# Optimization experiments

Measured on AMD Instinct MI355X. Metric: run time of the kernel, lower is better.

The kernel has to match this reference:

```python
import jax, jax.numpy as jnp
import numpy as np

D_MODEL = 512
NUM_HEADS = 8
D_HEAD = D_MODEL // NUM_HEADS
B, S = 2, 4096


def setup_inputs() -> dict:
    key = jax.random.key(0)
    ks = jax.random.split(key, 9)
    scale = 1.0 / np.sqrt(D_MODEL)
    x = jax.random.normal(ks[0], (B, S, D_MODEL), dtype=jnp.float32)
    Wq = jax.random.normal(ks[1], (D_MODEL, D_MODEL), dtype=jnp.float32) * scale
    Wk = jax.random.normal(ks[2], (D_MODEL, D_MODEL), dtype=jnp.float32) * scale
    Wv = jax.random.normal(ks[3], (D_MODEL, D_MODEL), dtype=jnp.float32) * scale
    Wo = jax.random.normal(ks[4], (D_MODEL, D_MODEL), dtype=jnp.float32) * scale
    bq = jnp.zeros((D_MODEL,), jnp.float32)
    bk = jnp.zeros((D_MODEL,), jnp.float32)
    bv = jnp.zeros((D_MODEL,), jnp.float32)
    bo = jnp.zeros((D_MODEL,), jnp.float32)
    return {"x": x, "Wq": Wq, "bq": bq, "Wk": Wk, "bk": bk,
            "Wv": Wv, "bv": bv, "Wo": Wo, "bo": bo}


def _split_heads(t):
    # [B, S, D] -> [B, H, S, d_head]
    b, s, _ = t.shape
    return t.reshape(b, s, NUM_HEADS, D_HEAD).transpose(0, 2, 1, 3)


def reference(x, Wq, bq, Wk, bk, Wv, bv, Wo, bo):
    q = _split_heads(x @ Wq + bq)  # [B,H,S,dh]
    k = _split_heads(x @ Wk + bk)
    v = _split_heads(x @ Wv + bv)
    scores = jnp.einsum("bhqd,bhkd->bhqk", q, k) / jnp.sqrt(
        jnp.asarray(D_HEAD, x.dtype))
    attn = jax.nn.softmax(scores, axis=-1)  # dropout is identity at inference
    out = jnp.einsum("bhqk,bhkd->bhqd", attn, v)  # [B,H,S,dh]
    out = out.transpose(0, 2, 1, 3).reshape(x.shape[0], x.shape[1], D_MODEL)
    return out @ Wo + bo
```

## Files before the change

### kernel.cpp

```cpp
#include <hip/hip_runtime.h>
#include <cstddef>

#define NB   2
#define SEQ  4096
#define DM   512
#define NH   8
#define DH   64
#define MTOT 8192
#define KSPLIT 2
#define KSEQ (SEQ / KSPLIT)

#define QSCALE 0.18033688011112042f

typedef __attribute__((ext_vector_type(8))) short short8;
typedef __attribute__((ext_vector_type(4))) float f32x4;

__device__ __forceinline__ ushort f2bf(float f) {
  unsigned u = __builtin_bit_cast(unsigned, f);
  u += 0x7FFFu + ((u >> 16) & 1u);
  return (ushort)(u >> 16);
}
__device__ __forceinline__ float bf2f(ushort b) {
  return __builtin_bit_cast(float, ((unsigned)b) << 16);
}
__device__ __forceinline__ unsigned cvt_pk_bf16(float lo, float hi) {
  unsigned r;
  asm("v_cvt_pk_bf16_f32 %0, %1, %2" : "=v"(r) : "v"(lo), "v"(hi));
  return r;
}
__device__ __forceinline__ float fexp2(float x) {
#if __has_builtin(__builtin_amdgcn_exp2f)
  return __builtin_amdgcn_exp2f(x);
#else
  float r;
  asm("v_exp_f32 %0, %1" : "=v"(r) : "v"(x));
  return r;
#endif
}

__global__ __launch_bounds__(256)
void prep_w_k(const float* __restrict__ Wq, const float* __restrict__ Wk,
              const float* __restrict__ Wv, const float* __restrict__ Wo,
              ushort* __restrict__ WTq, ushort* __restrict__ WTk,
              ushort* __restrict__ WTv, ushort* __restrict__ WTh,
              ushort* __restrict__ WTl) {
  const int z = blockIdx.z;
  const float* W = (z == 0) ? Wq : (z == 1) ? Wk : (z == 2) ? Wv : Wo;
  ushort* WT = (z == 0) ? WTq : (z == 1) ? WTk : (z == 2) ? WTv : WTh;
  ushort* WTlo = (z == 3) ? WTl : nullptr;

  __shared__ float t[32][33];
  const int k0 = blockIdx.x * 32, n0 = blockIdx.y * 32;
  const int tx = threadIdx.x & 31, ty = threadIdx.x >> 5;
#pragma unroll
  for (int i = 0; i < 32; i += 8)
    t[ty + i][tx] = W[(size_t)(k0 + ty + i) * DM + n0 + tx];
  __syncthreads();
#pragma unroll
  for (int i = 0; i < 32; i += 8) {
    float v = t[tx][ty + i];
    ushort h = f2bf(v);
    WT[(size_t)(n0 + ty + i) * DM + k0 + tx] = h;
    if (WTlo) WTlo[(size_t)(n0 + ty + i) * DM + k0 + tx] = f2bf(v - bf2f(h));
  }
}

__global__ __launch_bounds__(256)
void qkv_gemm_k(const float* __restrict__ x,
                const ushort* __restrict__ WTq, const ushort* __restrict__ WTk,
                const ushort* __restrict__ WTv,
                const float* __restrict__ bq, const float* __restrict__ bk,
                const float* __restrict__ bv,
                ushort* __restrict__ Qb, ushort* __restrict__ Kb,
                ushort* __restrict__ Vb) {
  __shared__ ushort smem[17408];
  ushort (*As)[40] = (ushort(*)[40])smem;
  ushort (*Bs)[40] = (ushort(*)[40])(smem + 5120);

  const int z = blockIdx.z;
  const ushort* WT = (z == 0) ? WTq : (z == 1) ? WTk : WTv;
  const float* bias = (z == 0) ? bq : (z == 1) ? bk : bv;
  ushort* outp = (z == 0) ? Qb : (z == 1) ? Kb : Vb;
  const float oscale = (z == 0) ? QSCALE : 1.0f;

  const int tid = threadIdx.x;
  const int w = tid >> 6, l = tid & 63;
  const int g = l >> 4, l15 = l & 15;
  const int wm = w >> 1, wn = w & 1;
  const int m0 = blockIdx.x * 128;
  const int n0 = blockIdx.y * 128;

  const int ar = tid >> 1, ac = (tid & 1) * 16;
  const float*  Ag = x  + (size_t)(m0 + ar) * DM + ac;
  const ushort* Bg = WT + (size_t)(n0 + ar) * DM + ac;

  float av[16];
#pragma unroll
  for (int i = 0; i < 16; i += 4)
    *(float4*)&av[i] = *(const float4*)(Ag + i);
  uint4 rb0 = *(const uint4*)(Bg);
  uint4 rb1 = *(const uint4*)(Bg + 8);

  float bfn[4];
#pragma unroll
  for (int fn = 0; fn < 4; ++fn)
    bfn[fn] = bias[n0 + wn * 64 + fn * 16 + l15];

  f32x4 acc[4][4];
#pragma unroll
  for (int fm = 0; fm < 4; ++fm)
#pragma unroll
    for (int fn = 0; fn < 4; ++fn) acc[fm][fn] = (f32x4){0.f, 0.f, 0.f, 0.f};

  for (int k0 = 0; k0 < DM; k0 += 32) {
    __syncthreads();
    {
      ushort hh[16];
#pragma unroll
      for (int i = 0; i < 16; ++i) hh[i] = f2bf(av[i]);
      *(uint4*)&As[ar][ac]     = *(const uint4*)&hh[0];
      *(uint4*)&As[ar][ac + 8] = *(const uint4*)&hh[8];
      *(uint4*)&Bs[ar][ac]     = rb0;
      *(uint4*)&Bs[ar][ac + 8] = rb1;
    }
    __syncthreads();
    if (k0 + 32 < DM) {
#pragma unroll
      for (int i = 0; i < 16; i += 4)
        *(float4*)&av[i] = *(const float4*)(Ag + k0 + 32 + i);
      rb0 = *(const uint4*)(Bg + k0 + 32);
      rb1 = *(const uint4*)(Bg + k0 + 40);
    }
    short8 af[4], bf[4];
#pragma unroll
    for (int fm = 0; fm < 4; ++fm)
      af[fm] = *(const short8*)&As[wm * 64 + fm * 16 + l15][g * 8];
#pragma unroll
    for (int fn = 0; fn < 4; ++fn)
      bf[fn] = *(const short8*)&Bs[wn * 64 + fn * 16 + l15][g * 8];
#pragma unroll
    for (int fm = 0; fm < 4; ++fm)
#pragma unroll
      for (int fn = 0; fn < 4; ++fn)
        acc[fm][fn] = __builtin_amdgcn_mfma_f32_16x16x32_bf16(
            af[fm], bf[fn], acc[fm][fn], 0, 0, 0);
  }

  if (z != 2) {
#pragma unroll
    for (int fm = 0; fm < 4; ++fm)
#pragma unroll
      for (int fn = 0; fn < 4; ++fn)
#pragma unroll
        for (int r = 0; r < 4; ++r) {
          int m = m0 + wm * 64 + fm * 16 + g * 4 + r;
          int n = n0 + wn * 64 + fn * 16 + l15;
          float v = (acc[fm][fn][r] + bfn[fn]) * oscale;
          int b = m >> 12, s = m & (SEQ - 1);
          int h = n >> 6, d = n & 63;
          outp[(size_t)((b * NH + h) * SEQ + s) * DH + d] = f2bf(v);
        }
  } else {
    __syncthreads();
    ushort (*T)[136] = (ushort(*)[136])smem;
#pragma unroll
    for (int fm = 0; fm < 4; ++fm)
#pragma unroll
      for (int fn = 0; fn < 4; ++fn)
#pragma unroll
        for (int r = 0; r < 4; ++r) {
          int ml = wm * 64 + fm * 16 + g * 4 + r;
          int nl = wn * 64 + fn * 16 + l15;
          T[nl][ml] = f2bf(acc[fm][fn][r] + bfn[fn]);
        }
    __syncthreads();
    const int b = m0 >> 12, s0 = m0 & (SEQ - 1);
#pragma unroll
    for (int it = 0; it < 8; ++it) {
      int ch = tid + 256 * it;
      int row = ch >> 4;
      int cc = (ch & 15) * 8;
      int n = n0 + row;
      int h = n >> 6, d = n & 63;
      *(uint4*)&outp[((size_t)(b * NH + h) * DH + d) * SEQ + s0 + cc] =
          *(const uint4*)&T[row][cc];
    }
  }
}

__global__ __launch_bounds__(256)
void oproj_gemm_k(const float* __restrict__ Po, const float* __restrict__ Dn,
                  const ushort* __restrict__ WTh, const ushort* __restrict__ WTl,
                  const float* __restrict__ bo, float* __restrict__ out) {
  __shared__ ushort Ah[128][40];
  __shared__ ushort Al[128][40];
  __shared__ ushort Bh[64][40];
  __shared__ ushort Bl[64][40];

  const int tid = threadIdx.x;
  const int w = tid >> 6, l = tid & 63;
  const int g = l >> 4, l15 = l & 15;
  const int wm = w >> 1, wn = w & 1;
  const int m0 = blockIdx.x * 128;
  const int n0 = blockIdx.y * 64;

  const int ar = tid >> 1, ac = (tid & 1) * 16;
  const int br = tid >> 2, bc = (tid & 3) * 8;

  const int m  = m0 + ar;
  const int bb = m >> 12, ss = m & (SEQ - 1);
  const size_t zoff = (size_t)(NB * NH) * SEQ * DH;

  const ushort* Bhg = WTh + (size_t)(n0 + br) * DM + bc;
  const ushort* Blg = WTl + (size_t)(n0 + br) * DM + bc;

  auto loadA = [&](int c, float* av) {
    const int h = c >> 6, d = c & 63;
    const int bh = bb * NH + h;
    const size_t i0 = ((size_t)bh * SEQ + ss) * DH + d;
    const float den = Dn[(size_t)bh * SEQ + ss] +
                      Dn[(size_t)(NB * NH + bh) * SEQ + ss];
    const float inv = __builtin_amdgcn_rcpf(den);
#pragma unroll
    for (int i = 0; i < 16; i += 4) {
      float4 p0 = *(const float4*)(Po + i0 + i);
      float4 p1 = *(const float4*)(Po + zoff + i0 + i);
      av[i + 0] = (p0.x + p1.x) * inv;
      av[i + 1] = (p0.y + p1.y) * inv;
      av[i + 2] = (p0.z + p1.z) * inv;
      av[i + 3] = (p0.w + p1.w) * inv;
    }
  };

  float av[16];
  loadA(ac, av);
  uint4 rbh = *(const uint4*)Bhg;
  uint4 rbl = *(const uint4*)Blg;

  float bfn[2];
#pragma unroll
  for (int fn = 0; fn < 2; ++fn)
    bfn[fn] = bo[n0 + wn * 32 + fn * 16 + l15];

  f32x4 acc[4][2];
#pragma unroll
  for (int fm = 0; fm < 4; ++fm)
#pragma unroll
    for (int fn = 0; fn < 2; ++fn) acc[fm][fn] = (f32x4){0.f, 0.f, 0.f, 0.f};

  for (int k0 = 0; k0 < DM; k0 += 32) {
    __syncthreads();
    {
      ushort hh[16], ll[16];
#pragma unroll
      for (int i = 0; i < 16; ++i) {
        ushort h = f2bf(av[i]);
        hh[i] = h;
        ll[i] = f2bf(av[i] - bf2f(h));
      }
      *(uint4*)&Ah[ar][ac]     = *(const uint4*)&hh[0];
      *(uint4*)&Ah[ar][ac + 8] = *(const uint4*)&hh[8];
      *(uint4*)&Al[ar][ac]     = *(const uint4*)&ll[0];
      *(uint4*)&Al[ar][ac + 8] = *(const uint4*)&ll[8];
      *(uint4*)&Bh[br][bc] = rbh;
      *(uint4*)&Bl[br][bc] = rbl;
    }
    __syncthreads();
    if (k0 + 32 < DM) {
      loadA(ac + k0 + 32, av);
      rbh = *(const uint4*)(Bhg + k0 + 32);
      rbl = *(const uint4*)(Blg + k0 + 32);
    }
    short8 ah[4], al[4], bh[2], bl[2];
#pragma unroll
    for (int fm = 0; fm < 4; ++fm) {
      ah[fm] = *(const short8*)&Ah[wm * 64 + fm * 16 + l15][g * 8];
      al[fm] = *(const short8*)&Al[wm * 64 + fm * 16 + l15][g * 8];
    }
#pragma unroll
    for (int fn = 0; fn < 2; ++fn) {
      bh[fn] = *(const short8*)&Bh[wn * 32 + fn * 16 + l15][g * 8];
      bl[fn] = *(const short8*)&Bl[wn * 32 + fn * 16 + l15][g * 8];
    }
#pragma unroll
    for (int fm = 0; fm < 4; ++fm)
#pragma unroll
      for (int fn = 0; fn < 2; ++fn) {
        f32x4 c = acc[fm][fn];
        c = __builtin_amdgcn_mfma_f32_16x16x32_bf16(ah[fm], bh[fn], c, 0, 0, 0);
        c = __builtin_amdgcn_mfma_f32_16x16x32_bf16(ah[fm], bl[fn], c, 0, 0, 0);
        c = __builtin_amdgcn_mfma_f32_16x16x32_bf16(al[fm], bh[fn], c, 0, 0, 0);
        acc[fm][fn] = c;
      }
  }

#pragma unroll
  for (int fm = 0; fm < 4; ++fm)
#pragma unroll
    for (int fn = 0; fn < 2; ++fn)
#pragma unroll
      for (int r = 0; r < 4; ++r) {
        int mm = m0 + wm * 64 + fm * 16 + g * 4 + r;
        int n = n0 + wn * 32 + fn * 16 + l15;
        out[(size_t)mm * DM + n] = acc[fm][fn][r] + bfn[fn];
      }
}

__global__ __launch_bounds__(256, 4)
void attn_mfma_k(const ushort* __restrict__ Q, const ushort* __restrict__ K,
                 const ushort* __restrict__ VT, float* __restrict__ Po,
                 float* __restrict__ Dn) {
  __shared__ ushort Ks[2][64][72];
  __shared__ unsigned Vt[2][64][36];

  const int tid = threadIdx.x;
  const int w   = tid >> 6;
  const int l   = tid & 63;
  const int g   = l >> 4;
  const int l15 = l & 15;
  const int bh  = blockIdx.y;
  const int z   = blockIdx.z;
  const int q0  = blockIdx.x * 128 + w * 32;
  const int tb  = z * KSEQ;

  short8 qb[2][2];
#pragma unroll
  for (int qh = 0; qh < 2; ++qh) {
    const ushort* Qrow = Q + ((size_t)bh * SEQ + q0 + qh * 16 + l15) * DH;
    qb[qh][0] = *(const short8*)(Qrow + g * 8);
    qb[qh][1] = *(const short8*)(Qrow + 32 + g * 8);
  }

  short8 vones;
#pragma unroll
  for (int i = 0; i < 8; ++i) vones[i] = (short)0x3F80;

  f32x4 acc[2][4];
  f32x4 accl[2];
#pragma unroll
  for (int qh = 0; qh < 2; ++qh) {
    accl[qh] = (f32x4){0.f, 0.f, 0.f, 0.f};
#pragma unroll
    for (int dt = 0; dt < 4; ++dt) acc[qh][dt] = (f32x4){0.f, 0.f, 0.f, 0.f};
  }

  const ushort* Kg = K + (size_t)bh * SEQ * DH;

  const int rho  = tid >> 2;
  const int kcol = (tid & 3) * 16;
  const int sig  = 32 * ((rho >> 5) & 1) + 8 * ((rho >> 2) & 3) +
                   4 * ((rho >> 4) & 1) + (rho & 3);
  const ushort* Kp = Kg + (size_t)(tb + sig) * DH + kcol;

  const int vrow = tid >> 2;
  const int vcb  = (tid & 3) * 8;
  const unsigned* Vrow =
      (const unsigned*)(VT + ((size_t)bh * DH + vrow) * SEQ) + tb / 2 + vcb;

  uint4 kr0 = *(const uint4*)(Kp);
  uint4 kr1 = *(const uint4*)(Kp + 8);
  uint4 vv0 = *(const uint4*)(Vrow);
  uint4 vv1 = *(const uint4*)(Vrow + 4);

  int cur = 0;
  for (int t0 = 0; t0 < KSEQ; t0 += 64) {
    *(uint4*)&Ks[cur][rho][kcol]     = kr0;
    *(uint4*)&Ks[cur][rho][kcol + 8] = kr1;
    *(uint4*)&Vt[cur][vrow][vcb]     = vv0;
    *(uint4*)&Vt[cur][vrow][vcb + 4] = vv1;
    if (t0 + 64 < KSEQ) {
      kr0 = *(const uint4*)(Kp + (size_t)(t0 + 64) * DH);
      kr1 = *(const uint4*)(Kp + (size_t)(t0 + 64) * DH + 8);
      vv0 = *(const uint4*)(Vrow + (t0 + 64) / 2);
      vv1 = *(const uint4*)(Vrow + (t0 + 64) / 2 + 4);
    }
    __syncthreads();

    f32x4 s[2][4];
    __builtin_amdgcn_s_setprio(1);
#pragma unroll
    for (int nf = 0; nf < 4; ++nf) {
      short8 ka0 = *(const short8*)&Ks[cur][nf * 16 + l15][g * 8];
      short8 ka1 = *(const short8*)&Ks[cur][nf * 16 + l15][32 + g * 8];
#pragma unroll
      for (int qh = 0; qh < 2; ++qh) {
        f32x4 c = (f32x4){0.f, 0.f, 0.f, 0.f};
        c = __builtin_amdgcn_mfma_f32_16x16x32_bf16(ka0, qb[qh][0], c, 0, 0, 0);
        c = __builtin_amdgcn_mfma_f32_16x16x32_bf16(ka1, qb[qh][1], c, 0, 0, 0);
        s[qh][nf] = c;
      }
    }
    __builtin_amdgcn_s_setprio(0);

    short8 pa[2][2];
#pragma unroll
    for (int qh = 0; qh < 2; ++qh) {
      float p[4][4];
#pragma unroll
      for (int nf = 0; nf < 4; ++nf)
#pragma unroll
        for (int r = 0; r < 4; ++r) p[nf][r] = fexp2(s[qh][nf][r]);
      uint4 u0, u1;
      u0.x = cvt_pk_bf16(p[0][0], p[0][1]);
      u0.y = cvt_pk_bf16(p[0][2], p[0][3]);
      u0.z = cvt_pk_bf16(p[1][0], p[1][1]);
      u0.w = cvt_pk_bf16(p[1][2], p[1][3]);
      u1.x = cvt_pk_bf16(p[2][0], p[2][1]);
      u1.y = cvt_pk_bf16(p[2][2], p[2][3]);
      u1.z = cvt_pk_bf16(p[3][0], p[3][1]);
      u1.w = cvt_pk_bf16(p[3][2], p[3][3]);
      pa[qh][0] = __builtin_bit_cast(short8, u0);
      pa[qh][1] = __builtin_bit_cast(short8, u1);
    }

    __builtin_amdgcn_s_setprio(1);
#pragma unroll
    for (int dt = 0; dt < 4; ++dt) {
      short8 vb0 = *(const short8*)&Vt[cur][dt * 16 + l15][4 * g];
      short8 vb1 = *(const short8*)&Vt[cur][dt * 16 + l15][16 + 4 * g];
#pragma unroll
      for (int qh = 0; qh < 2; ++qh) {
        acc[qh][dt] = __builtin_amdgcn_mfma_f32_16x16x32_bf16(pa[qh][0], vb0,
                                                              acc[qh][dt], 0, 0, 0);
        acc[qh][dt] = __builtin_amdgcn_mfma_f32_16x16x32_bf16(pa[qh][1], vb1,
                                                              acc[qh][dt], 0, 0, 0);
      }
    }
#pragma unroll
    for (int qh = 0; qh < 2; ++qh) {
      accl[qh] = __builtin_amdgcn_mfma_f32_16x16x32_bf16(pa[qh][0], vones,
                                                         accl[qh], 0, 0, 0);
      accl[qh] = __builtin_amdgcn_mfma_f32_16x16x32_bf16(pa[qh][1], vones,
                                                         accl[qh], 0, 0, 0);
    }
    __builtin_amdgcn_s_setprio(0);
    cur ^= 1;
  }

  const int zo = z * (NB * NH) + bh;
#pragma unroll
  for (int qh = 0; qh < 2; ++qh) {
#pragma unroll
    for (int dt = 0; dt < 4; ++dt)
#pragma unroll
      for (int r = 0; r < 4; ++r) {
        int srow = q0 + qh * 16 + g * 4 + r;
        Po[((size_t)zo * SEQ + srow) * DH + dt * 16 + l15] = acc[qh][dt][r];
      }
    if (l15 == 0)
#pragma unroll
      for (int r = 0; r < 4; ++r)
        Dn[(size_t)zo * SEQ + q0 + qh * 16 + g * 4 + r] = accl[qh][r];
  }
}

extern "C" void kernel_launch(void* const* d_in, const int* in_sizes, int n_in,
                              void* d_out, int out_size, void* d_ws, size_t ws_size,
                              hipStream_t stream) {
  const float* x  = (const float*)d_in[0];
  const float* Wq = (const float*)d_in[1];
  const float* bq = (const float*)d_in[2];
  const float* Wk = (const float*)d_in[3];
  const float* bk = (const float*)d_in[4];
  const float* Wv = (const float*)d_in[5];
  const float* bv = (const float*)d_in[6];
  const float* Wo = (const float*)d_in[7];
  const float* bo = (const float*)d_in[8];
  float* out = (float*)d_out;

  const size_t per = (size_t)NB * NH * SEQ * DH;
  const size_t wsz = (size_t)DM * DM;
  ushort* WTq = (ushort*)d_ws;
  ushort* WTk = WTq + wsz;
  ushort* WTv = WTk + wsz;
  ushort* WTh = WTv + wsz;
  ushort* WTl = WTh + wsz;
  ushort* Qb  = WTl + wsz;
  ushort* Kb  = Qb + per;
  ushort* Vb  = Kb + per;
  float*  Po  = (float*)(Vb + per);
  float*  Dn  = Po + (size_t)KSPLIT * per;

  prep_w_k<<<dim3(16, 16, 4), 256, 0, stream>>>(Wq, Wk, Wv, Wo,
                                                WTq, WTk, WTv, WTh, WTl);
  qkv_gemm_k<<<dim3(MTOT / 128, DM / 128, 3), 256, 0, stream>>>(
      x, WTq, WTk, WTv, bq, bk, bv, Qb, Kb, Vb);
  attn_mfma_k<<<dim3(SEQ / 128, NB * NH, KSPLIT), 256, 0, stream>>>(
      Qb, Kb, Vb, Po, Dn);
  oproj_gemm_k<<<dim3(MTOT / 128, DM / 64), 256, 0, stream>>>(
      Po, Dn, WTh, WTl, bo, out);
}
```

Baseline: 145.1 us.

## Precast GEMM A-operands to bf16 in separate kernels before QKV and output projection

Adds a kernel that converts x to bf16 once, so the QKV GEMM (gridded over 3 weights and 4 column tiles) no longer rereads fp32 x and reconverts it in every block. Adds a combine kernel that merges the two split-K attention partials, normalizes them and splits the result into bf16 hi/lo arrays, which the output projection then loads directly. Each GEMM A tile is re-read across many column blocks, so doing the conversion once is meant to cut redundant global reads and conversion ALU work. In exchange it adds two launches and extra workspace round trips, and the hi/lo buffers reuse the xb and Qb regions.

```diff
diff --git a/kernel.cpp b/kernel.cpp
--- a/kernel.cpp
+++ b/kernel.cpp
@@ -36,6 +36,16 @@
   asm("v_exp_f32 %0, %1" : "=v"(r) : "v"(x));
   return r;
 #endif
+}
+
+__global__ __launch_bounds__(256)
+void xcast_k(const float* __restrict__ x, ushort* __restrict__ xb) {
+  const int i = (blockIdx.x * 256 + threadIdx.x) * 8;
+  float4 a = *(const float4*)(x + i);
+  float4 b = *(const float4*)(x + i + 4);
+  ushort h[8] = {f2bf(a.x), f2bf(a.y), f2bf(a.z), f2bf(a.w),
+                 f2bf(b.x), f2bf(b.y), f2bf(b.z), f2bf(b.w)};
+  *(uint4*)(xb + i) = *(const uint4*)h;
 }
 
 __global__ __launch_bounds__(256)
@@ -66,7 +76,7 @@
 }
 
 __global__ __launch_bounds__(256)
-void qkv_gemm_k(const float* __restrict__ x,
+void qkv_gemm_k(const ushort* __restrict__ xb,
                 const ushort* __restrict__ WTq, const ushort* __restrict__ WTk,
                 const ushort* __restrict__ WTv,
                 const float* __restrict__ bq, const float* __restrict__ bk,
@@ -91,13 +101,11 @@
   const int n0 = blockIdx.y * 128;
 
   const int ar = tid >> 1, ac = (tid & 1) * 16;
-  const float*  Ag = x  + (size_t)(m0 + ar) * DM + ac;
+  const ushort* Ag = xb + (size_t)(m0 + ar) * DM + ac;
   const ushort* Bg = WT + (size_t)(n0 + ar) * DM + ac;
 
-  float av[16];
-#pragma unroll
-  for (int i = 0; i < 16; i += 4)
-    *(float4*)&av[i] = *(const float4*)(Ag + i);
+  uint4 ra0 = *(const uint4*)(Ag);
+  uint4 ra1 = *(const uint4*)(Ag + 8);
   uint4 rb0 = *(const uint4*)(Bg);
   uint4 rb1 = *(const uint4*)(Bg + 8);
 
@@ -114,20 +122,14 @@
 
   for (int k0 = 0; k0 < DM; k0 += 32) {
     __syncthreads();
-    {
-      ushort hh[16];
-#pragma unroll
-      for (int i = 0; i < 16; ++i) hh[i] = f2bf(av[i]);
-      *(uint4*)&As[ar][ac]     = *(const uint4*)&hh[0];
-      *(uint4*)&As[ar][ac + 8] = *(const uint4*)&hh[8];
-      *(uint4*)&Bs[ar][ac]     = rb0;
-      *(uint4*)&Bs[ar][ac + 8] = rb1;
-    }
+    *(uint4*)&As[ar][ac]     = ra0;
+    *(uint4*)&As[ar][ac + 8] = ra1;
+    *(uint4*)&Bs[ar][ac]     = rb0;
+    *(uint4*)&Bs[ar][ac + 8] = rb1;
     __syncthreads();
     if (k0 + 32 < DM) {
-#pragma unroll
-      for (int i = 0; i < 16; i += 4)
-        *(float4*)&av[i] = *(const float4*)(Ag + k0 + 32 + i);
+      ra0 = *(const uint4*)(Ag + k0 + 32);
+      ra1 = *(const uint4*)(Ag + k0 + 40);
       rb0 = *(const uint4*)(Bg + k0 + 32);
       rb1 = *(const uint4*)(Bg + k0 + 40);
     }
@@ -189,7 +191,39 @@
 }
 
 __global__ __launch_bounds__(256)
-void oproj_gemm_k(const float* __restrict__ Po, const float* __restrict__ Dn,
+void combine_k(const float* __restrict__ Po, const float* __restrict__ Dn,
+               ushort* __restrict__ Ahb, ushort* __restrict__ Alb) {
+  const size_t o = (size_t)(blockIdx.x * 256 + threadIdx.x) * 8;
+  const int m = (int)(o >> 9);
+  const int c = (int)(o & 511);
+  const int b = m >> 12, s = m & (SEQ - 1);
+  const int h = c >> 6, d = c & 63;
+  const int bh = b * NH + h;
+  const size_t i0 = ((size_t)bh * SEQ + s) * DH + d;
+  const size_t zoff = (size_t)(NB * NH) * SEQ * DH;
+  const float den = Dn[(size_t)bh * SEQ + s] +
+                    Dn[(size_t)(NB * NH + bh) * SEQ + s];
+  const float inv = __builtin_amdgcn_rcpf(den);
+  ushort hh[8], ll[8];
+#pragma unroll
+  for (int i = 0; i < 8; i += 4) {
+    float4 p0 = *(const float4*)(Po + i0 + i);
+    float4 p1 = *(const float4*)(Po + zoff + i0 + i);
+    float v[4] = {(p0.x + p1.x) * inv, (p0.y + p1.y) * inv,
+                  (p0.z + p1.z) * inv, (p0.w + p1.w) * inv};
+#pragma unroll
+    for (int j = 0; j < 4; ++j) {
+      ushort hb = f2bf(v[j]);
+      hh[i + j] = hb;
+      ll[i + j] = f2bf(v[j] - bf2f(hb));
+    }
+  }
+  *(uint4*)(Ahb + o) = *(const uint4*)hh;
+  *(uint4*)(Alb + o) = *(const uint4*)ll;
+}
+
+__global__ __launch_bounds__(256)
+void oproj_gemm_k(const ushort* __restrict__ Ahb, const ushort* __restrict__ Alb,
                   const ushort* __restrict__ WTh, const ushort* __restrict__ WTl,
                   const float* __restrict__ bo, float* __restrict__ out) {
   __shared__ ushort Ah[128][40];
@@ -207,33 +241,15 @@
   const int ar = tid >> 1, ac = (tid & 1) * 16;
   const int br = tid >> 2, bc = (tid & 3) * 8;
 
-  const int m  = m0 + ar;
-  const int bb = m >> 12, ss = m & (SEQ - 1);
-  const size_t zoff = (size_t)(NB * NH) * SEQ * DH;
-
+  const ushort* Ahg = Ahb + (size_t)(m0 + ar) * DM + ac;
+  const ushort* Alg = Alb + (size_t)(m0 + ar) * DM + ac;
   const ushort* Bhg = WTh + (size_t)(n0 + br) * DM + bc;
   const ushort* Blg = WTl + (size_t)(n0 + br) * DM + bc;
 
-  auto loadA = [&](int c, float* av) {
-    const int h = c >> 6, d = c & 63;
-    const int bh = bb * NH + h;
-    const size_t i0 = ((size_t)bh * SEQ + ss) * DH + d;
-    const float den = Dn[(size_t)bh * SEQ + ss] +
-                      Dn[(size_t)(NB * NH + bh) * SEQ + ss];
-    const float inv = __builtin_amdgcn_rcpf(den);
-#pragma unroll
-    for (int i = 0; i < 16; i += 4) {
-      float4 p0 = *(const float4*)(Po + i0 + i);
-      float4 p1 = *(const float4*)(Po + zoff + i0 + i);
-      av[i + 0] = (p0.x + p1.x) * inv;
-      av[i + 1] = (p0.y + p1.y) * inv;
-      av[i + 2] = (p0.z + p1.z) * inv;
-      av[i + 3] = (p0.w + p1.w) * inv;
-    }
-  };
-
-  float av[16];
-  loadA(ac, av);
+  uint4 rah0 = *(const uint4*)(Ahg);
+  uint4 rah1 = *(const uint4*)(Ahg + 8);
+  uint4 ral0 = *(const uint4*)(Alg);
+  uint4 ral1 = *(const uint4*)(Alg + 8);
   uint4 rbh = *(const uint4*)Bhg;
   uint4 rbl = *(const uint4*)Blg;
 
@@ -250,24 +266,18 @@
 
   for (int k0 = 0; k0 < DM; k0 += 32) {
     __syncthreads();
-    {
-      ushort hh[16], ll[16];
-#pragma unroll
-      for (int i = 0; i < 16; ++i) {
-        ushort h = f2bf(av[i]);
-        hh[i] = h;
-        ll[i] = f2bf(av[i] - bf2f(h));
-      }
-      *(uint4*)&Ah[ar][ac]     = *(const uint4*)&hh[0];
-      *(uint4*)&Ah[ar][ac + 8] = *(const uint4*)&hh[8];
-      *(uint4*)&Al[ar][ac]     = *(const uint4*)&ll[0];
-      *(uint4*)&Al[ar][ac + 8] = *(const uint4*)&ll[8];
-      *(uint4*)&Bh[br][bc] = rbh;
-      *(uint4*)&Bl[br][bc] = rbl;
-    }
+    *(uint4*)&Ah[ar][ac]     = rah0;
+    *(uint4*)&Ah[ar][ac + 8] = rah1;
+    *(uint4*)&Al[ar][ac]     = ral0;
+    *(uint4*)&Al[ar][ac + 8] = ral1;
+    *(uint4*)&Bh[br][bc] = rbh;
+    *(uint4*)&Bl[br][bc] = rbl;
     __syncthreads();
     if (k0 + 32 < DM) {
-      loadA(ac + k0 + 32, av);
+      rah0 = *(const uint4*)(Ahg + k0 + 32);
+      rah1 = *(const uint4*)(Ahg + k0 + 40);
+      ral0 = *(const uint4*)(Alg + k0 + 32);
+      ral1 = *(const uint4*)(Alg + k0 + 40);
       rbh = *(const uint4*)(Bhg + k0 + 32);
       rbl = *(const uint4*)(Blg + k0 + 32);
     }
@@ -470,7 +480,8 @@
 
   const size_t per = (size_t)NB * NH * SEQ * DH;
   const size_t wsz = (size_t)DM * DM;
-  ushort* WTq = (ushort*)d_ws;
+  ushort* xb  = (ushort*)d_ws;
+  ushort* WTq = xb + (size_t)MTOT * DM;
   ushort* WTk = WTq + wsz;
   ushort* WTv = WTk + wsz;
   ushort* WTh = WTv + wsz;
@@ -480,13 +491,17 @@
   ushort* Vb  = Kb + per;
   float*  Po  = (float*)(Vb + per);
   float*  Dn  = Po + (size_t)KSPLIT * per;
-
+  ushort* Ahb = xb;
+  ushort* Alb = Qb;
+
+  xcast_k<<<MTOT * DM / (256 * 8), 256, 0, stream>>>(x, xb);
   prep_w_k<<<dim3(16, 16, 4), 256, 0, stream>>>(Wq, Wk, Wv, Wo,
                                                 WTq, WTk, WTv, WTh, WTl);
   qkv_gemm_k<<<dim3(MTOT / 128, DM / 128, 3), 256, 0, stream>>>(
-      x, WTq, WTk, WTv, bq, bk, bv, Qb, Kb, Vb);
+      xb, WTq, WTk, WTv, bq, bk, bv, Qb, Kb, Vb);
   attn_mfma_k<<<dim3(SEQ / 128, NB * NH, KSPLIT), 256, 0, stream>>>(
       Qb, Kb, Vb, Po, Dn);
+  combine_k<<<MTOT * DM / (256 * 8), 256, 0, stream>>>(Po, Dn, Ahb, Alb);
   oproj_gemm_k<<<dim3(MTOT / 128, DM / 64), 256, 0, stream>>>(
-      Po, Dn, WTh, WTl, bo, out);
-}
+      Ahb, Alb, WTh, WTl, bo, out);
+}
```

After: 141.7 us. 1.02x faster.
